# Kernel tuning notes

Measured on AMD Instinct MI355X. Metric: run time of the kernel, lower is better.

The kernel has to match this reference:

```python
import jax, jax.numpy as jnp
import numpy as np
from jax import lax

B, T, F, H, D = 16384, 79, 3, 256, 256  # batch, levels, n_input_fields, rnn_channels, dense_width


def setup_inputs() -> dict:
    key = jax.random.key(0)
    ks = jax.random.split(key, 8)
    return {
        "x0": jax.random.normal(ks[0], (B, T), dtype=jnp.float32),
        "x1": jax.random.normal(ks[1], (B, T), dtype=jnp.float32),
        "x2": jax.random.normal(ks[2], (B, T), dtype=jnp.float32),
        # SimpleRNN params: kernel [F,H], recurrent kernel [H,H] (scaled small so relu recurrence stays stable), bias [H]
        "W_in": jax.random.normal(ks[3], (F, H), dtype=jnp.float32) * 0.1,
        "U": jax.random.normal(ks[4], (H, H), dtype=jnp.float32) * 0.05,
        "b_rnn": jnp.zeros((H,), dtype=jnp.float32),
        # MLPBlock depth=1: single Dense(D)
        "W_d": jax.random.normal(ks[5], (H, D), dtype=jnp.float32) * 0.05,
        "b_d": jnp.zeros((D,), dtype=jnp.float32),
    }


def reference(x0, x1, x2, W_in, U, b_rnn, W_d, b_d):
    # CombineInputs(-1, expand=True): stack fields on new trailing axis -> [B, T, F]
    x = jnp.stack([x0, x1, x2], axis=-1)
    # go_backwards=True: SimpleRNN consumes the sequence in reverse order
    x = x[:, ::-1, :]
    # Batched input projection (hoisted out of the recurrence): [B, T, H]
    xp = jnp.einsum("btf,fh->bth", x, W_in) + b_rnn
    xp_t = jnp.swapaxes(xp, 0, 1)  # [T, B, H] for scan over time

    def step(h, xt):
        h = jax.nn.relu(xt + h @ U)
        return h, None

    h0 = jnp.zeros((x.shape[0], W_in.shape[1]), dtype=x.dtype)
    hT, _ = lax.scan(step, h0, xp_t)  # final hidden state [B, H]
    # MLPBlock(depth=1, combine_inputs=False): single Dense, no activation
    return hT @ W_d + b_d
```

## Files before the change

### kernel.cpp

```cpp
#include <hip/hip_runtime.h>
#include <hip/hip_bf16.h>
#include <stdint.h>

#define Bsz   16384
#define Tt    79
#define Hh    256
#define Dd    256
#define KP    288
#define LROW  296
#define NTILE 32
#define THR   256

typedef __attribute__((ext_vector_type(8))) short  short8;
typedef __attribute__((ext_vector_type(4))) float  float4_;

__device__ __forceinline__ unsigned short f2bf(float f){
  unsigned u = __float_as_uint(f);
  u += 0x7fffu + ((u >> 16) & 1u);
  return (unsigned short)(u >> 16);
}
__device__ __forceinline__ unsigned pk2(float a, float b){
  __hip_bfloat162 h = __float22bfloat162_rn(make_float2(a, b));
  return *(unsigned*)&h;
}

__global__ void build_tables(const float* __restrict__ W_in,
                             const float* __restrict__ U,
                             const float* __restrict__ b_rnn,
                             const float* __restrict__ W_d,
                             const float* __restrict__ b_d,
                             unsigned short* __restrict__ Ut,
                             unsigned short* __restrict__ Wdt){
  const int TBL = 256 * KP;
  int idx = blockIdx.x * 256 + threadIdx.x;
  if (idx >= 2 * TBL) return;
  int tb  = idx / TBL;
  int rem = idx - tb * TBL;
  int m = rem / KP;
  int k = rem - m * KP;
  float v = 0.f;
  if (tb == 0){
    if      (k < 256) v = U[k * 256 + m];
    else if (k < 259) v = W_in[(k - 256) * 256 + m];
    else if (k == 259) v = b_rnn[m];
  } else {
    if      (k < 256) v = W_d[k * 256 + m];
    else if (k == 259) v = b_d[m];
  }
  unsigned short o = f2bf(v);
  if (tb == 0) Ut[rem] = o; else Wdt[rem] = o;
}

__global__ __launch_bounds__(THR, 2) void rnn_main(
    const float* __restrict__ x0,
    const float* __restrict__ x1,
    const float* __restrict__ x2,
    const unsigned short* __restrict__ Ut,
    const unsigned short* __restrict__ Wdt,
    float* __restrict__ out){
  __shared__ __align__(16) short hbuf[2][NTILE * LROW];

  const int tid  = threadIdx.x;
  const int lane = tid & 63;
  const int wm   = tid >> 6;
  const int quad = lane >> 4;
  const int ln   = lane & 15;
  const int qoff = quad * 8;
  const int bbase = blockIdx.x * NTILE;
  const int rb0 = ln;
  const int rb1 = ln + 16;

  {
    int4* p = (int4*)&hbuf[0][0];
    const int tot = 2 * NTILE * LROW * 2 / 16;
    int4 z = make_int4(0, 0, 0, 0);
    for (int i = tid; i < tot; i += THR) p[i] = z;
  }
  __syncthreads();

  if (tid < NTILE){
    hbuf[0][tid * LROW + 259] = (short)0x3F80;
    hbuf[1][tid * LROW + 259] = (short)0x3F80;
  }

  const bool stager = (wm == 0) && (lane < NTILE);
  const int  sn  = lane & (NTILE - 1);
  const int  sgb = bbase + sn;
  if (stager){
    int tr = Tt - 1;
    float a = x0[sgb * Tt + tr];
    float b = x1[sgb * Tt + tr];
    float c = x2[sgb * Tt + tr];
    *(unsigned*)&hbuf[0][sn * LROW + 256] = pk2(a, b);
    hbuf[0][sn * LROW + 258] = (short)f2bf(c);
  }

  short8 afr[4][9];
  #pragma unroll
  for (int mt = 0; mt < 4; ++mt){
    const unsigned short* p = Ut + (wm * 64 + mt * 16 + ln) * KP + qoff;
    #pragma unroll
    for (int kt = 0; kt < 9; ++kt){
      afr[mt][kt] = *(const short8*)(p + kt * 32);
    }
  }

  __syncthreads();

  const float4_ zz = {0.f, 0.f, 0.f, 0.f};
  float4_ acc[4][2];

  #pragma unroll 1
  for (int t = 0; t < Tt; ++t){
    float xa = 0.f, xb = 0.f, xc = 0.f;
    if (stager && t < Tt - 1){
      int tr = Tt - 2 - t;
      xa = x0[sgb * Tt + tr];
      xb = x1[sgb * Tt + tr];
      xc = x2[sgb * Tt + tr];
    }

    const short* hb = &hbuf[t & 1][0];
    short*       hw = &hbuf[(t + 1) & 1][0];

    #pragma unroll
    for (int kt = 0; kt < 9; ++kt){
      short8 b0 = *(const short8*)&hb[rb0 * LROW + kt * 32 + qoff];
      short8 b1 = *(const short8*)&hb[rb1 * LROW + kt * 32 + qoff];
      #pragma unroll
      for (int mt = 0; mt < 4; ++mt){
        if (kt == 0){
          acc[mt][0] = __builtin_amdgcn_mfma_f32_16x16x32_bf16(afr[mt][0], b0, zz, 0, 0, 0);
          acc[mt][1] = __builtin_amdgcn_mfma_f32_16x16x32_bf16(afr[mt][0], b1, zz, 0, 0, 0);
        } else {
          acc[mt][0] = __builtin_amdgcn_mfma_f32_16x16x32_bf16(afr[mt][kt], b0, acc[mt][0], 0, 0, 0);
          acc[mt][1] = __builtin_amdgcn_mfma_f32_16x16x32_bf16(afr[mt][kt], b1, acc[mt][1], 0, 0, 0);
        }
      }
    }

    #pragma unroll
    for (int mt = 0; mt < 4; ++mt){
      #pragma unroll
      for (int nt = 0; nt < 2; ++nt){
        float4_ v = acc[mt][nt];
        uint2 w;
        w.x = pk2(fmaxf(v[0], 0.f), fmaxf(v[1], 0.f));
        w.y = pk2(fmaxf(v[2], 0.f), fmaxf(v[3], 0.f));
        int n = nt * 16 + ln;
        int m = wm * 64 + mt * 16 + quad * 4;
        *(uint2*)&hw[n * LROW + m] = w;
      }
    }
    if (stager && t < Tt - 1){
      *(unsigned*)&hw[sn * LROW + 256] = pk2(xa, xb);
      hw[sn * LROW + 258] = (short)f2bf(xc);
    }

    __syncthreads();
  }

  const short* hb = &hbuf[Tt & 1][0];
  float4_ oacc[4][2];
  #pragma unroll
  for (int kt = 0; kt < 9; ++kt){
    short8 wf[4];
    #pragma unroll
    for (int mt = 0; mt < 4; ++mt){
      int m = wm * 64 + mt * 16 + ln;
      wf[mt] = *(const short8*)(Wdt + m * KP + kt * 32 + qoff);
    }
    short8 b0 = *(const short8*)&hb[rb0 * LROW + kt * 32 + qoff];
    short8 b1 = *(const short8*)&hb[rb1 * LROW + kt * 32 + qoff];
    #pragma unroll
    for (int mt = 0; mt < 4; ++mt){
      if (kt == 0){
        oacc[mt][0] = __builtin_amdgcn_mfma_f32_16x16x32_bf16(wf[mt], b0, zz, 0, 0, 0);
        oacc[mt][1] = __builtin_amdgcn_mfma_f32_16x16x32_bf16(wf[mt], b1, zz, 0, 0, 0);
      } else {
        oacc[mt][0] = __builtin_amdgcn_mfma_f32_16x16x32_bf16(wf[mt], b0, oacc[mt][0], 0, 0, 0);
        oacc[mt][1] = __builtin_amdgcn_mfma_f32_16x16x32_bf16(wf[mt], b1, oacc[mt][1], 0, 0, 0);
      }
    }
  }

  #pragma unroll
  for (int mt = 0; mt < 4; ++mt){
    #pragma unroll
    for (int nt = 0; nt < 2; ++nt){
      int n = nt * 16 + ln;
      int m = wm * 64 + mt * 16 + quad * 4;
      *(float4_*)&out[(bbase + n) * Dd + m] = oacc[mt][nt];
    }
  }
}

extern "C" void kernel_launch(void* const* d_in, const int* in_sizes, int n_in,
                              void* d_out, int out_size, void* d_ws, size_t ws_size,
                              hipStream_t stream){
  const float* x0    = (const float*)d_in[0];
  const float* x1    = (const float*)d_in[1];
  const float* x2    = (const float*)d_in[2];
  const float* W_in  = (const float*)d_in[3];
  const float* U     = (const float*)d_in[4];
  const float* b_rnn = (const float*)d_in[5];
  const float* W_d   = (const float*)d_in[6];
  const float* b_d   = (const float*)d_in[7];

  unsigned short* Ut  = (unsigned short*)d_ws;
  unsigned short* Wdt = Ut + 256 * KP;
  float* out = (float*)d_out;

  build_tables<<<(2 * 256 * KP + 255) / 256, 256, 0, stream>>>(W_in, U, b_rnn, W_d, b_d, Ut, Wdt);
  rnn_main<<<Bsz / NTILE, THR, 0, stream>>>(x0, x1, x2, Ut, Wdt, out);
}
```

Before: 214.3 us.

## Switch recurrence and output GEMMs to 32x32x16 MFMA with tighter K padding

Replaces the 16x16x32 bf16 MFMA tiling with 32x32x16 MFMA, so each wave computes two 32x32 output tiles per step from a single shared B fragment. K padding shrinks from 288 to 272 (17 k-steps of 16), which cuts padded MFMA work and LDS traffic. The time loop is unrolled by two so the ping-pong buffer pointers become fixed, and the x staging loads are spread across all four waves. The trade-off is only two independent accumulator chains per wave, so back-to-back dependent MFMA latency may be exposed.

After: 223.2 us. +4.2%, slower.

```diff
diff --git a/kernel.cpp b/kernel.cpp
--- a/kernel.cpp
+++ b/kernel.cpp
@@ -4,15 +4,15 @@
 
 #define Bsz   16384
 #define Tt    79
-#define Hh    256
 #define Dd    256
-#define KP    288
-#define LROW  296
+#define KP    272
+#define LROW  280
 #define NTILE 32
 #define THR   256
 
-typedef __attribute__((ext_vector_type(8))) short  short8;
-typedef __attribute__((ext_vector_type(4))) float  float4_;
+typedef __attribute__((ext_vector_type(8)))  short short8;
+typedef __attribute__((ext_vector_type(4)))  float float4_;
+typedef __attribute__((ext_vector_type(16))) float float16_;
 
 __device__ __forceinline__ unsigned short f2bf(float f){
   unsigned u = __float_as_uint(f);
@@ -63,12 +63,10 @@
   const int tid  = threadIdx.x;
   const int lane = tid & 63;
   const int wm   = tid >> 6;
-  const int quad = lane >> 4;
-  const int ln   = lane & 15;
-  const int qoff = quad * 8;
+  const int nl   = lane & 31;
+  const int hi   = lane >> 5;
+  const int hi8  = hi * 8;
   const int bbase = blockIdx.x * NTILE;
-  const int rb0 = ln;
-  const int rb1 = ln + 16;
 
   {
     int4* p = (int4*)&hbuf[0][0];
@@ -83,8 +81,8 @@
     hbuf[1][tid * LROW + 259] = (short)0x3F80;
   }
 
-  const bool stager = (wm == 0) && (lane < NTILE);
-  const int  sn  = lane & (NTILE - 1);
+  const bool stager = (lane < 8);
+  const int  sn  = wm * 8 + (lane & 7);
   const int  sgb = bbase + sn;
   if (stager){
     int tr = Tt - 1;
@@ -95,103 +93,90 @@
     hbuf[0][sn * LROW + 258] = (short)f2bf(c);
   }
 
-  short8 afr[4][9];
+  short8 afr[2][17];
   #pragma unroll
-  for (int mt = 0; mt < 4; ++mt){
-    const unsigned short* p = Ut + (wm * 64 + mt * 16 + ln) * KP + qoff;
+  for (int mt = 0; mt < 2; ++mt){
+    const unsigned short* p = Ut + (wm * 64 + mt * 32 + nl) * KP + hi8;
     #pragma unroll
-    for (int kt = 0; kt < 9; ++kt){
-      afr[mt][kt] = *(const short8*)(p + kt * 32);
+    for (int kt = 0; kt < 17; ++kt){
+      afr[mt][kt] = *(const short8*)(p + kt * 16);
     }
   }
 
   __syncthreads();
 
-  const float4_ zz = {0.f, 0.f, 0.f, 0.f};
-  float4_ acc[4][2];
-
-  #pragma unroll 1
-  for (int t = 0; t < Tt; ++t){
+  const float16_ zz16 = {0.f,0.f,0.f,0.f,0.f,0.f,0.f,0.f,
+                         0.f,0.f,0.f,0.f,0.f,0.f,0.f,0.f};
+
+  auto step = [&](const short* __restrict__ hb, short* __restrict__ hw, int t){
     float xa = 0.f, xb = 0.f, xc = 0.f;
-    if (stager && t < Tt - 1){
+    const bool pf = stager && (t < Tt - 1);
+    if (pf){
       int tr = Tt - 2 - t;
       xa = x0[sgb * Tt + tr];
       xb = x1[sgb * Tt + tr];
       xc = x2[sgb * Tt + tr];
     }
 
-    const short* hb = &hbuf[t & 1][0];
-    short*       hw = &hbuf[(t + 1) & 1][0];
-
+    float16_ a0, a1;
     #pragma unroll
-    for (int kt = 0; kt < 9; ++kt){
-      short8 b0 = *(const short8*)&hb[rb0 * LROW + kt * 32 + qoff];
-      short8 b1 = *(const short8*)&hb[rb1 * LROW + kt * 32 + qoff];
-      #pragma unroll
-      for (int mt = 0; mt < 4; ++mt){
-        if (kt == 0){
-          acc[mt][0] = __builtin_amdgcn_mfma_f32_16x16x32_bf16(afr[mt][0], b0, zz, 0, 0, 0);
-          acc[mt][1] = __builtin_amdgcn_mfma_f32_16x16x32_bf16(afr[mt][0], b1, zz, 0, 0, 0);
-        } else {
-          acc[mt][0] = __builtin_amdgcn_mfma_f32_16x16x32_bf16(afr[mt][kt], b0, acc[mt][0], 0, 0, 0);
-          acc[mt][1] = __builtin_amdgcn_mfma_f32_16x16x32_bf16(afr[mt][kt], b1, acc[mt][1], 0, 0, 0);
-        }
+    for (int kt = 0; kt < 17; ++kt){
+      short8 b = *(const short8*)&hb[nl * LROW + kt * 16 + hi8];
+      if (kt == 0){
+        a0 = __builtin_amdgcn_mfma_f32_32x32x16_bf16(afr[0][0], b, zz16, 0, 0, 0);
+        a1 = __builtin_amdgcn_mfma_f32_32x32x16_bf16(afr[1][0], b, zz16, 0, 0, 0);
+      } else {
+        a0 = __builtin_amdgcn_mfma_f32_32x32x16_bf16(afr[0][kt], b, a0, 0, 0, 0);
+        a1 = __builtin_amdgcn_mfma_f32_32x32x16_bf16(afr[1][kt], b, a1, 0, 0, 0);
       }
     }
 
     #pragma unroll
-    for (int mt = 0; mt < 4; ++mt){
-      #pragma unroll
-      for (int nt = 0; nt < 2; ++nt){
-        float4_ v = acc[mt][nt];
-        uint2 w;
-        w.x = pk2(fmaxf(v[0], 0.f), fmaxf(v[1], 0.f));
-        w.y = pk2(fmaxf(v[2], 0.f), fmaxf(v[3], 0.f));
-        int n = nt * 16 + ln;
-        int m = wm * 64 + mt * 16 + quad * 4;
-        *(uint2*)&hw[n * LROW + m] = w;
-      }
-    }
-    if (stager && t < Tt - 1){
+    for (int g = 0; g < 4; ++g){
+      uint2 w;
+      w.x = pk2(fmaxf(a0[4*g+0], 0.f), fmaxf(a0[4*g+1], 0.f));
+      w.y = pk2(fmaxf(a0[4*g+2], 0.f), fmaxf(a0[4*g+3], 0.f));
+      *(uint2*)&hw[nl * LROW + wm * 64 +      8 * g + 4 * hi] = w;
+      w.x = pk2(fmaxf(a1[4*g+0], 0.f), fmaxf(a1[4*g+1], 0.f));
+      w.y = pk2(fmaxf(a1[4*g+2], 0.f), fmaxf(a1[4*g+3], 0.f));
+      *(uint2*)&hw[nl * LROW + wm * 64 + 32 + 8 * g + 4 * hi] = w;
+    }
+    if (pf){
       *(unsigned*)&hw[sn * LROW + 256] = pk2(xa, xb);
       hw[sn * LROW + 258] = (short)f2bf(xc);
     }
-
     __syncthreads();
-  }
-
-  const short* hb = &hbuf[Tt & 1][0];
-  float4_ oacc[4][2];
+  };
+
+  #pragma unroll 1
+  for (int t = 0; t < Tt - 1; t += 2){
+    step(&hbuf[0][0], &hbuf[1][0], t);
+    step(&hbuf[1][0], &hbuf[0][0], t + 1);
+  }
+  step(&hbuf[0][0], &hbuf[1][0], Tt - 1);
+
+  const short* hb = &hbuf[1][0];
+  float16_ o0, o1;
   #pragma unroll
-  for (int kt = 0; kt < 9; ++kt){
-    short8 wf[4];
-    #pragma unroll
-    for (int mt = 0; mt < 4; ++mt){
-      int m = wm * 64 + mt * 16 + ln;
-      wf[mt] = *(const short8*)(Wdt + m * KP + kt * 32 + qoff);
-    }
-    short8 b0 = *(const short8*)&hb[rb0 * LROW + kt * 32 + qoff];
-    short8 b1 = *(const short8*)&hb[rb1 * LROW + kt * 32 + qoff];
-    #pragma unroll
-    for (int mt = 0; mt < 4; ++mt){
-      if (kt == 0){
-        oacc[mt][0] = __builtin_amdgcn_mfma_f32_16x16x32_bf16(wf[mt], b0, zz, 0, 0, 0);
-        oacc[mt][1] = __builtin_amdgcn_mfma_f32_16x16x32_bf16(wf[mt], b1, zz, 0, 0, 0);
-      } else {
-        oacc[mt][0] = __builtin_amdgcn_mfma_f32_16x16x32_bf16(wf[mt], b0, oacc[mt][0], 0, 0, 0);
-        oacc[mt][1] = __builtin_amdgcn_mfma_f32_16x16x32_bf16(wf[mt], b1, oacc[mt][1], 0, 0, 0);
-      }
-    }
-  }
-
+  for (int kt = 0; kt < 17; ++kt){
+    short8 w0 = *(const short8*)(Wdt + (wm * 64 +      nl) * KP + kt * 16 + hi8);
+    short8 w1 = *(const short8*)(Wdt + (wm * 64 + 32 + nl) * KP + kt * 16 + hi8);
+    short8 b  = *(const short8*)&hb[nl * LROW + kt * 16 + hi8];
+    if (kt == 0){
+      o0 = __builtin_amdgcn_mfma_f32_32x32x16_bf16(w0, b, zz16, 0, 0, 0);
+      o1 = __builtin_amdgcn_mfma_f32_32x32x16_bf16(w1, b, zz16, 0, 0, 0);
+    } else {
+      o0 = __builtin_amdgcn_mfma_f32_32x32x16_bf16(w0, b, o0, 0, 0, 0);
+      o1 = __builtin_amdgcn_mfma_f32_32x32x16_bf16(w1, b, o1, 0, 0, 0);
+    }
+  }
   #pragma unroll
-  for (int mt = 0; mt < 4; ++mt){
-    #pragma unroll
-    for (int nt = 0; nt < 2; ++nt){
-      int n = nt * 16 + ln;
-      int m = wm * 64 + mt * 16 + quad * 4;
-      *(float4_*)&out[(bbase + n) * Dd + m] = oacc[mt][nt];
-    }
+  for (int g = 0; g < 4; ++g){
+    int m0 = wm * 64 + 8 * g + 4 * hi;
+    float4_ v0 = {o0[4*g+0], o0[4*g+1], o0[4*g+2], o0[4*g+3]};
+    float4_ v1 = {o1[4*g+0], o1[4*g+1], o1[4*g+2], o1[4*g+3]};
+    *(float4_*)&out[(bbase + nl) * Dd + m0]      = v0;
+    *(float4_*)&out[(bbase + nl) * Dd + m0 + 32] = v1;
   }
 }
 
```
